# Kernel optimization log

Hardware: AMD Instinct MI355X
Metric: run time of the kernel (lower is better)

## Reference

```python
import jax, jax.numpy as jnp
import numpy as np

INPUT_SIZE = 512
HIDDEN_SIZE = 512
BATCH = 16384


def setup_inputs() -> dict:
    key = jax.random.key(0)
    ks = jax.random.split(key, 11)
    stdv = 1.0 / np.sqrt(HIDDEN_SIZE)
    in_dim = INPUT_SIZE + HIDDEN_SIZE

    def unif(k, shape):
        return jax.random.uniform(k, shape, jnp.float32, -stdv, stdv)

    inp = {
        "input_": jax.random.normal(ks[0], (BATCH, INPUT_SIZE), jnp.float32),
        "prev_h": jax.random.normal(ks[1], (BATCH, HIDDEN_SIZE), jnp.float32),
        "prev_c": jax.random.normal(ks[2], (BATCH, HIDDEN_SIZE), jnp.float32),
        # gate weights in torch nn.Linear layout: (out=hidden, in=input+hidden)
        "W_i": unif(ks[3], (HIDDEN_SIZE, in_dim)),
        "b_i": unif(ks[4], (HIDDEN_SIZE,)),
        "W_f": unif(ks[5], (HIDDEN_SIZE, in_dim)),
        "b_f": unif(ks[6], (HIDDEN_SIZE,)),
        "W_g": unif(ks[7], (HIDDEN_SIZE, in_dim)),
        "b_g": unif(ks[8], (HIDDEN_SIZE,)),
        "W_o": unif(ks[9], (HIDDEN_SIZE, in_dim)),
        "b_o": unif(ks[10], (HIDDEN_SIZE,)),
    }
    return inp


def reference(input_, prev_h, prev_c, W_i, b_i, W_f, b_f, W_g, b_g, W_o, b_o):
    # x_stack = cat((prev_h, input_), dim=1)  -> (batch, hidden+input)
    x_stack = jnp.concatenate([prev_h, input_], axis=1)
    # Fuse the four gate GEMMs into one: stack weights along out dim.
    W = jnp.concatenate([W_i, W_f, W_o, W_g], axis=0)          # (4H, H+I)
    b = jnp.concatenate([b_i, b_f, b_o, b_g], axis=0)          # (4H,)
    gates = x_stack @ W.T + b                                   # (batch, 4H)
    H = prev_h.shape[1]
    i = jax.nn.sigmoid(gates[:, 0 * H:1 * H])
    f = jax.nn.sigmoid(gates[:, 1 * H:2 * H])
    o = jax.nn.sigmoid(gates[:, 2 * H:3 * H])
    g = jnp.tanh(gates[:, 3 * H:4 * H])
    c = f * prev_c + i * g
    h = jnp.tanh(c) * o
    return (h, c)
```

## Files before the change

kernel.cpp:

```cpp
#include <hip/hip_runtime.h>
#include <hip/hip_bf16.h>
#include <math.h>

typedef unsigned short u16;

#define BATCH 16384
#define HID   512
#define KDIM  1024
#define BM    128
#define BN    32
#define BK    64

typedef __bf16 bf16x8 __attribute__((ext_vector_type(8)));
typedef float  floatx4 __attribute__((ext_vector_type(4)));

__device__ __forceinline__ void async_copy16(const void* g, void* l) {
  __builtin_amdgcn_global_load_lds(
      (const __attribute__((address_space(1))) void*)g,
      (__attribute__((address_space(3))) void*)l, 16, 0, 0);
}

__device__ __forceinline__ float fast_sigmoid(float x) {
  return 1.0f / (1.0f + __expf(-x));
}
__device__ __forceinline__ float fast_tanh(float x) {
  float e = __expf(-2.0f * fabsf(x));
  float t = (1.0f - e) / (1.0f + e);
  return x >= 0.0f ? t : -t;
}
__device__ __forceinline__ u16 f2bf(float f) {
  return __builtin_bit_cast(u16, __float2bfloat16(f));
}

__global__ __launch_bounds__(256) void pack_kernel(
    const float* __restrict__ input_, const float* __restrict__ prev_h,
    const float* __restrict__ Wi, const float* __restrict__ Wf,
    const float* __restrict__ Wo, const float* __restrict__ Wg,
    u16* __restrict__ Xb, u16* __restrict__ Wb) {
  int blk = blockIdx.x;
  int col = threadIdx.x * 4;
  const float* src;
  u16* dst;
  if (blk < BATCH) {
    src = (col < HID) ? (prev_h + (size_t)blk * HID + col)
                      : (input_ + (size_t)blk * HID + (col - HID));
    dst = Xb + (size_t)blk * KDIM + col;
  } else {
    int grow = blk - BATCH;
    int gate = grow >> 9;
    int n = grow & (HID - 1);
    const float* s = gate == 0 ? Wi : gate == 1 ? Wf : gate == 2 ? Wo : Wg;
    src = s + (size_t)n * KDIM + col;
    dst = Wb + (size_t)grow * KDIM + col;
  }
  float4 v = *(const float4*)src;
  ushort4 o;
  o.x = f2bf(v.x); o.y = f2bf(v.y); o.z = f2bf(v.z); o.w = f2bf(v.w);
  *(ushort4*)dst = o;
}

__global__ __launch_bounds__(256) void lstm_gemm_kernel(
    const u16* __restrict__ Xb, const u16* __restrict__ Wb,
    const float* __restrict__ Bi, const float* __restrict__ Bf,
    const float* __restrict__ Bo, const float* __restrict__ Bg,
    const float* __restrict__ prevC, float* __restrict__ out) {
  __shared__ u16 lds[16384];

  const int tid = threadIdx.x;
  const int wave = tid >> 6, lane = tid & 63;
  const int lrow = lane & 15, lquad = lane >> 4;
  const int m_block = blockIdx.x * BM;
  const int n_block = blockIdx.y * BN;
  const int m_off = (wave >> 1) * 64;
  const int n_off = (wave & 1) * 16;

  const int swz = ((lane & 7) ^ (lane >> 3)) * 8;
  const u16* gp[8];
  u16* lp[8];
#pragma unroll
  for (int i = 0; i < 8; ++i) {
    int li = wave * 8 + i;
    if (li < 16) {
      int row = m_block + li * 8 + (lane >> 3);
      gp[i] = Xb + (size_t)row * KDIM + swz;
      lp[i] = &lds[li * 512];
    } else {
      int br = (li - 16) * 8 + (lane >> 3);
      int grow = (br >> 5) * HID + n_block + (br & 31);
      gp[i] = Wb + (size_t)grow * KDIM + swz;
      lp[i] = &lds[8192 + (li - 16) * 512];
    }
  }

  floatx4 acc[4][4];
#pragma unroll
  for (int g = 0; g < 4; ++g)
#pragma unroll
    for (int mt = 0; mt < 4; ++mt)
      acc[g][mt] = (floatx4){0.f, 0.f, 0.f, 0.f};

  const int rswz = (lrow & 7);

  for (int k0 = 0; k0 < KDIM; k0 += BK) {
    __syncthreads();
#pragma unroll
    for (int i = 0; i < 8; ++i)
      async_copy16(gp[i] + k0, lp[i]);
    __syncthreads();

#pragma unroll
    for (int kk = 0; kk < 2; ++kk) {
      const int c = kk * 4 + lquad;
      const int ak = (c ^ rswz) * 8;
      bf16x8 a[4], b[4];
#pragma unroll
      for (int mt = 0; mt < 4; ++mt)
        a[mt] = *(const bf16x8*)&lds[(m_off + mt * 16 + lrow) * 64 + ak];
#pragma unroll
      for (int g = 0; g < 4; ++g)
        b[g] = *(const bf16x8*)&lds[8192 + (g * 32 + n_off + lrow) * 64 + ak];
#pragma unroll
      for (int g = 0; g < 4; ++g)
#pragma unroll
        for (int mt = 0; mt < 4; ++mt)
          acc[g][mt] = __builtin_amdgcn_mfma_f32_16x16x32_bf16(
              a[mt], b[g], acc[g][mt], 0, 0, 0);
    }
  }

  const int j = n_block + n_off + lrow;
  const float vbi = Bi[j], vbf = Bf[j], vbo = Bo[j], vbg = Bg[j];
  float* outH = out;
  float* outC = out + (size_t)BATCH * HID;
#pragma unroll
  for (int mt = 0; mt < 4; ++mt) {
    int rowb = m_block + m_off + mt * 16 + lquad * 4;
#pragma unroll
    for (int r = 0; r < 4; ++r) {
      int row = rowb + r;
      float gi = fast_sigmoid(acc[0][mt][r] + vbi);
      float gf = fast_sigmoid(acc[1][mt][r] + vbf);
      float go = fast_sigmoid(acc[2][mt][r] + vbo);
      float gg = fast_tanh(acc[3][mt][r] + vbg);
      float c = gf * prevC[row * HID + j] + gi * gg;
      float h = fast_tanh(c) * go;
      outH[row * HID + j] = h;
      outC[row * HID + j] = c;
    }
  }
}

__global__ void lstm_fallback_kernel(
    const float* __restrict__ input_, const float* __restrict__ prev_h,
    const float* __restrict__ prevC,
    const float* __restrict__ Wi, const float* __restrict__ Bi,
    const float* __restrict__ Wf, const float* __restrict__ Bf,
    const float* __restrict__ Wo, const float* __restrict__ Bo,
    const float* __restrict__ Wg, const float* __restrict__ Bg,
    float* __restrict__ out) {
  int idx = blockIdx.x * blockDim.x + threadIdx.x;
  int b = idx / HID, j = idx % HID;
  if (b >= BATCH) return;
  float si = 0.f, sf = 0.f, so = 0.f, sg = 0.f;
  for (int k = 0; k < KDIM; ++k) {
    float x = (k < HID) ? prev_h[b * HID + k] : input_[b * HID + (k - HID)];
    si += x * Wi[j * KDIM + k];
    sf += x * Wf[j * KDIM + k];
    so += x * Wo[j * KDIM + k];
    sg += x * Wg[j * KDIM + k];
  }
  float gi = fast_sigmoid(si + Bi[j]);
  float gf = fast_sigmoid(sf + Bf[j]);
  float go = fast_sigmoid(so + Bo[j]);
  float gg = fast_tanh(sg + Bg[j]);
  float c = gf * prevC[b * HID + j] + gi * gg;
  out[b * HID + j] = fast_tanh(c) * go;
  out[(size_t)BATCH * HID + b * HID + j] = c;
}

extern "C" void kernel_launch(void* const* d_in, const int* in_sizes, int n_in,
                              void* d_out, int out_size, void* d_ws, size_t ws_size,
                              hipStream_t stream) {
  const float* input_ = (const float*)d_in[0];
  const float* prev_h = (const float*)d_in[1];
  const float* prev_c = (const float*)d_in[2];
  const float* W_i = (const float*)d_in[3];
  const float* b_i = (const float*)d_in[4];
  const float* W_f = (const float*)d_in[5];
  const float* b_f = (const float*)d_in[6];
  const float* W_g = (const float*)d_in[7];
  const float* b_g = (const float*)d_in[8];
  const float* W_o = (const float*)d_in[9];
  const float* b_o = (const float*)d_in[10];
  float* out = (float*)d_out;

  const size_t ws_needed =
      (size_t)BATCH * KDIM * sizeof(u16) + (size_t)4 * HID * KDIM * sizeof(u16);

  if (ws_size < ws_needed) {
    int total = BATCH * HID;
    lstm_fallback_kernel<<<(total + 255) / 256, 256, 0, stream>>>(
        input_, prev_h, prev_c, W_i, b_i, W_f, b_f, W_o, b_o, W_g, b_g, out);
    return;
  }

  u16* Xb = (u16*)d_ws;
  u16* Wb = Xb + (size_t)BATCH * KDIM;

  pack_kernel<<<BATCH + 4 * HID, 256, 0, stream>>>(input_, prev_h,
                                                   W_i, W_f, W_o, W_g, Xb, Wb);

  dim3 grid(BATCH / BM, HID / BN);
  lstm_gemm_kernel<<<grid, 256, 0, stream>>>(Xb, Wb, b_i, b_f, b_o, b_g,
                                             prev_c, out);
}
```

Baseline: 244.7 us.

## Enlarge GEMM tiles to 256x64 per gate with double-buffered LDS pipeline

The LSTM GEMM kernel now uses 512-thread blocks covering 256 batch rows by 64 hidden columns per gate, with BK reduced to 32. The LDS is split into two buffers so async global-to-LDS copies for the next k-slice are issued before computing the current one, overlapping loads with MFMA work. Larger tiles raise data reuse per block and cut the grid size. The cost is higher register pressure (32 accumulator tiles per wave), a new swizzle pattern and fewer blocks per CU.

Result: no change. 248.6 us (+1.6%).

```diff
diff --git a/kernel.cpp b/kernel.cpp
--- a/kernel.cpp
+++ b/kernel.cpp
@@ -7,9 +7,9 @@
 #define BATCH 16384
 #define HID   512
 #define KDIM  1024
-#define BM    128
-#define BN    32
-#define BK    64
+#define BM    256
+#define BNG   64
+#define BK    32
 
 typedef __bf16 bf16x8 __attribute__((ext_vector_type(8)));
 typedef float  floatx4 __attribute__((ext_vector_type(4)));
@@ -59,93 +59,109 @@
   *(ushort4*)dst = o;
 }
 
-__global__ __launch_bounds__(256) void lstm_gemm_kernel(
+__global__ __launch_bounds__(512, 2) void lstm_gemm_kernel(
     const u16* __restrict__ Xb, const u16* __restrict__ Wb,
     const float* __restrict__ Bi, const float* __restrict__ Bf,
     const float* __restrict__ Bo, const float* __restrict__ Bg,
     const float* __restrict__ prevC, float* __restrict__ out) {
-  __shared__ u16 lds[16384];
+  __shared__ u16 lds[2][16384];
 
   const int tid = threadIdx.x;
   const int wave = tid >> 6, lane = tid & 63;
   const int lrow = lane & 15, lquad = lane >> 4;
   const int m_block = blockIdx.x * BM;
-  const int n_block = blockIdx.y * BN;
+  const int nb = blockIdx.y * BNG;
   const int m_off = (wave >> 1) * 64;
-  const int n_off = (wave & 1) * 16;
-
-  const int swz = ((lane & 7) ^ (lane >> 3)) * 8;
-  const u16* gp[8];
-  u16* lp[8];
-#pragma unroll
-  for (int i = 0; i < 8; ++i) {
-    int li = wave * 8 + i;
-    if (li < 16) {
-      int row = m_block + li * 8 + (lane >> 3);
-      gp[i] = Xb + (size_t)row * KDIM + swz;
-      lp[i] = &lds[li * 512];
+  const int n_off = (wave & 1) * 32;
+
+  const int swz = (((lane & 3) ^ ((lane >> 2) & 3)) * 8);
+  const u16* gp[4];
+  int lp[4];
+#pragma unroll
+  for (int i = 0; i < 4; ++i) {
+    int base = wave * 32 + (i & 1) * 16;
+    int r = base + (lane >> 2);
+    if (i < 2) {
+      gp[i] = Xb + (size_t)(m_block + r) * KDIM + swz;
+      lp[i] = base * 32;
     } else {
-      int br = (li - 16) * 8 + (lane >> 3);
-      int grow = (br >> 5) * HID + n_block + (br & 31);
-      gp[i] = Wb + (size_t)grow * KDIM + swz;
-      lp[i] = &lds[8192 + (li - 16) * 512];
+      int gate = r >> 6, col = r & 63;
+      gp[i] = Wb + (size_t)(gate * HID + nb + col) * KDIM + swz;
+      lp[i] = 8192 + base * 32;
     }
   }
 
-  floatx4 acc[4][4];
+  floatx4 acc[4][2][4];
 #pragma unroll
   for (int g = 0; g < 4; ++g)
 #pragma unroll
+    for (int nt = 0; nt < 2; ++nt)
+#pragma unroll
+      for (int mt = 0; mt < 4; ++mt)
+        acc[g][nt][mt] = (floatx4){0.f, 0.f, 0.f, 0.f};
+
+  const int roff = ((lquad ^ (lrow & 3)) * 8);
+
+  auto fill = [&](int buf, int k0) {
+#pragma unroll
+    for (int i = 0; i < 4; ++i)
+      async_copy16(gp[i] + k0, &lds[0][0] + buf * 16384 + lp[i]);
+  };
+
+  auto compute = [&](int buf) {
+    const u16* LA = &lds[buf][0];
+    const u16* LB = &lds[buf][8192];
+    bf16x8 a[4], b[4][2];
+#pragma unroll
     for (int mt = 0; mt < 4; ++mt)
-      acc[g][mt] = (floatx4){0.f, 0.f, 0.f, 0.f};
-
-  const int rswz = (lrow & 7);
-
-  for (int k0 = 0; k0 < KDIM; k0 += BK) {
+      a[mt] = *(const bf16x8*)&LA[(m_off + mt * 16 + lrow) * 32 + roff];
+#pragma unroll
+    for (int g = 0; g < 4; ++g)
+#pragma unroll
+      for (int nt = 0; nt < 2; ++nt)
+        b[g][nt] = *(const bf16x8*)
+            &LB[(g * 64 + n_off + nt * 16 + lrow) * 32 + roff];
+#pragma unroll
+    for (int g = 0; g < 4; ++g)
+#pragma unroll
+      for (int nt = 0; nt < 2; ++nt)
+#pragma unroll
+        for (int mt = 0; mt < 4; ++mt)
+          acc[g][nt][mt] = __builtin_amdgcn_mfma_f32_16x16x32_bf16(
+              a[mt], b[g][nt], acc[g][nt][mt], 0, 0, 0);
+  };
+
+  fill(0, 0);
+  for (int k0 = 0; k0 < KDIM; k0 += 2 * BK) {
     __syncthreads();
-#pragma unroll
-    for (int i = 0; i < 8; ++i)
-      async_copy16(gp[i] + k0, lp[i]);
+    fill(1, k0 + BK);
+    compute(0);
     __syncthreads();
-
-#pragma unroll
-    for (int kk = 0; kk < 2; ++kk) {
-      const int c = kk * 4 + lquad;
-      const int ak = (c ^ rswz) * 8;
-      bf16x8 a[4], b[4];
-#pragma unroll
-      for (int mt = 0; mt < 4; ++mt)
-        a[mt] = *(const bf16x8*)&lds[(m_off + mt * 16 + lrow) * 64 + ak];
-#pragma unroll
-      for (int g = 0; g < 4; ++g)
-        b[g] = *(const bf16x8*)&lds[8192 + (g * 32 + n_off + lrow) * 64 + ak];
-#pragma unroll
-      for (int g = 0; g < 4; ++g)
-#pragma unroll
-        for (int mt = 0; mt < 4; ++mt)
-          acc[g][mt] = __builtin_amdgcn_mfma_f32_16x16x32_bf16(
-              a[mt], b[g], acc[g][mt], 0, 0, 0);
-    }
-  }
-
-  const int j = n_block + n_off + lrow;
-  const float vbi = Bi[j], vbf = Bf[j], vbo = Bo[j], vbg = Bg[j];
+    if (k0 + 2 * BK < KDIM) fill(0, k0 + 2 * BK);
+    compute(1);
+  }
+
   float* outH = out;
   float* outC = out + (size_t)BATCH * HID;
 #pragma unroll
-  for (int mt = 0; mt < 4; ++mt) {
-    int rowb = m_block + m_off + mt * 16 + lquad * 4;
-#pragma unroll
-    for (int r = 0; r < 4; ++r) {
-      int row = rowb + r;
-      float gi = fast_sigmoid(acc[0][mt][r] + vbi);
-      float gf = fast_sigmoid(acc[1][mt][r] + vbf);
-      float go = fast_sigmoid(acc[2][mt][r] + vbo);
-      float gg = fast_tanh(acc[3][mt][r] + vbg);
-      float c = gf * prevC[row * HID + j] + gi * gg;
-      float h = fast_tanh(c) * go;
-      outH[row * HID + j] = h;
-      outC[row * HID + j] = c;
+  for (int nt = 0; nt < 2; ++nt) {
+    const int j = nb + n_off + nt * 16 + lrow;
+    const float vbi = Bi[j], vbf = Bf[j], vbo = Bo[j], vbg = Bg[j];
+#pragma unroll
+    for (int mt = 0; mt < 4; ++mt) {
+      int rowb = m_block + m_off + mt * 16 + lquad * 4;
+#pragma unroll
+      for (int r = 0; r < 4; ++r) {
+        int row = rowb + r;
+        float gi = fast_sigmoid(acc[0][nt][mt][r] + vbi);
+        float gf = fast_sigmoid(acc[1][nt][mt][r] + vbf);
+        float go = fast_sigmoid(acc[2][nt][mt][r] + vbo);
+        float gg = fast_tanh(acc[3][nt][mt][r] + vbg);
+        float c = gf * prevC[row * HID + j] + gi * gg;
+        float h = fast_tanh(c) * go;
+        outH[row * HID + j] = h;
+        outC[row * HID + j] = c;
+      }
     }
   }
 }
@@ -210,7 +226,7 @@
   pack_kernel<<<BATCH + 4 * HID, 256, 0, stream>>>(input_, prev_h,
                                                    W_i, W_f, W_o, W_g, Xb, Wb);
 
-  dim3 grid(BATCH / BM, HID / BN);
-  lstm_gemm_kernel<<<grid, 256, 0, stream>>>(Xb, Wb, b_i, b_f, b_o, b_g,
+  dim3 grid(BATCH / BM, HID / BNG);
+  lstm_gemm_kernel<<<grid, 512, 0, stream>>>(Xb, Wb, b_i, b_f, b_o, b_g,
                                              prev_c, out);
 }
```

## Pre-swizzle weights into MFMA fragment layout and double-buffer A tiles

Applied to the files above, without the earlier changes.

The pack kernel now writes bf16 weights in an MFMA-fragment-ordered layout, so each wave loads B operands directly from global memory into registers instead of staging them through LDS. The GEMM kernel moves to 512-thread blocks covering 128 rows by 128 hidden columns across all four gates, with each wave owning a 16-column slice and 8 M tiles. Only the X tile goes through LDS, now double-buffered so the next K step's copy overlaps the current MFMA work. The cost is much higher register pressure (128 accumulator floats plus prefetched B fragments) and heavy reliance on L2 for weight reuse across blocks.

Result: no change. 241.1 us (-1.4%).

```diff
diff --git a/kernel.cpp b/kernel.cpp
--- a/kernel.cpp
+++ b/kernel.cpp
@@ -8,8 +8,8 @@
 #define HID   512
 #define KDIM  1024
 #define BM    128
-#define BN    32
-#define BK    64
+#define BNG   128
+#define NSTEP 16
 
 typedef __bf16 bf16x8 __attribute__((ext_vector_type(8)));
 typedef float  floatx4 __attribute__((ext_vector_type(4)));
@@ -34,107 +34,117 @@
 
 __global__ __launch_bounds__(256) void pack_kernel(
     const float* __restrict__ input_, const float* __restrict__ prev_h,
-    const float* __restrict__ Wi, const float* __restrict__ Wf,
+    const float* __restrict__ Wi, const float* __restrict__ Wf_,
     const float* __restrict__ Wo, const float* __restrict__ Wg,
-    u16* __restrict__ Xb, u16* __restrict__ Wb) {
+    u16* __restrict__ Xb, u16* __restrict__ Wf) {
   int blk = blockIdx.x;
-  int col = threadIdx.x * 4;
-  const float* src;
-  u16* dst;
+  int k = threadIdx.x * 4;
   if (blk < BATCH) {
-    src = (col < HID) ? (prev_h + (size_t)blk * HID + col)
-                      : (input_ + (size_t)blk * HID + (col - HID));
-    dst = Xb + (size_t)blk * KDIM + col;
+    const float* src = (k < HID) ? (prev_h + (size_t)blk * HID + k)
+                                 : (input_ + (size_t)blk * HID + (k - HID));
+    float4 v = *(const float4*)src;
+    ushort4 o;
+    o.x = f2bf(v.x); o.y = f2bf(v.y); o.z = f2bf(v.z); o.w = f2bf(v.w);
+    *(ushort4*)(Xb + (size_t)blk * KDIM + k) = o;
   } else {
     int grow = blk - BATCH;
-    int gate = grow >> 9;
+    int g = grow >> 9;
     int n = grow & (HID - 1);
-    const float* s = gate == 0 ? Wi : gate == 1 ? Wf : gate == 2 ? Wo : Wg;
-    src = s + (size_t)n * KDIM + col;
-    dst = Wb + (size_t)grow * KDIM + col;
-  }
-  float4 v = *(const float4*)src;
-  ushort4 o;
-  o.x = f2bf(v.x); o.y = f2bf(v.y); o.z = f2bf(v.z); o.w = f2bf(v.w);
-  *(ushort4*)dst = o;
-}
-
-__global__ __launch_bounds__(256) void lstm_gemm_kernel(
-    const u16* __restrict__ Xb, const u16* __restrict__ Wb,
+    const float* s = g == 0 ? Wi : g == 1 ? Wf_ : g == 2 ? Wo : Wg;
+    float4 v = *(const float4*)(s + (size_t)n * KDIM + k);
+    ushort4 o;
+    o.x = f2bf(v.x); o.y = f2bf(v.y); o.z = f2bf(v.z); o.w = f2bf(v.w);
+    size_t d = ((size_t)((g * 32 + (n >> 4)) * 32 + (k >> 5)) * 64 +
+                ((k >> 3) & 3) * 16 + (n & 15)) * 8 + (k & 7);
+    *(ushort4*)(Wf + d) = o;
+  }
+}
+
+__global__ __launch_bounds__(512, 2) void lstm_gemm_kernel(
+    const u16* __restrict__ Xb, const u16* __restrict__ Wf,
     const float* __restrict__ Bi, const float* __restrict__ Bf,
     const float* __restrict__ Bo, const float* __restrict__ Bg,
     const float* __restrict__ prevC, float* __restrict__ out) {
-  __shared__ u16 lds[16384];
+  __shared__ u16 lds[2][8192];
 
   const int tid = threadIdx.x;
   const int wave = tid >> 6, lane = tid & 63;
   const int lrow = lane & 15, lquad = lane >> 4;
   const int m_block = blockIdx.x * BM;
-  const int n_block = blockIdx.y * BN;
-  const int m_off = (wave >> 1) * 64;
-  const int n_off = (wave & 1) * 16;
-
-  const int swz = ((lane & 7) ^ (lane >> 3)) * 8;
-  const u16* gp[8];
-  u16* lp[8];
-#pragma unroll
-  for (int i = 0; i < 8; ++i) {
-    int li = wave * 8 + i;
-    if (li < 16) {
-      int row = m_block + li * 8 + (lane >> 3);
-      gp[i] = Xb + (size_t)row * KDIM + swz;
-      lp[i] = &lds[li * 512];
-    } else {
-      int br = (li - 16) * 8 + (lane >> 3);
-      int grow = (br >> 5) * HID + n_block + (br & 31);
-      gp[i] = Wb + (size_t)grow * KDIM + swz;
-      lp[i] = &lds[8192 + (li - 16) * 512];
+  const int ntg = blockIdx.y * 8 + wave;
+
+  const int swz = ((lane & 7) ^ ((lane >> 3) & 7)) * 8;
+  const u16* gp[2];
+  int lp[2];
+#pragma unroll
+  for (int i = 0; i < 2; ++i) {
+    int li = wave * 2 + i;
+    gp[i] = Xb + (size_t)(m_block + li * 8 + (lane >> 3)) * KDIM + swz;
+    lp[i] = li * 512;
+  }
+
+  floatx4 acc[4][8];
+#pragma unroll
+  for (int g = 0; g < 4; ++g)
+#pragma unroll
+    for (int mt = 0; mt < 8; ++mt)
+      acc[g][mt] = (floatx4){0.f, 0.f, 0.f, 0.f};
+
+  auto fill = [&](int buf, int S) {
+#pragma unroll
+    for (int i = 0; i < 2; ++i)
+      async_copy16(gp[i] + S * 64, &lds[0][0] + buf * 8192 + lp[i]);
+  };
+
+  auto loadB = [&](int S, bf16x8 (&dst)[2][4]) {
+#pragma unroll
+    for (int kk = 0; kk < 2; ++kk)
+#pragma unroll
+      for (int g = 0; g < 4; ++g)
+        dst[kk][g] = *(const bf16x8*)(
+            Wf + (((size_t)(g * 32 + ntg) * 32 + (S * 2 + kk)) << 9) +
+            lane * 8);
+  };
+
+  auto compute = [&](int buf, bf16x8 (&B)[2][4]) {
+    const u16* LA = &lds[buf][0];
+#pragma unroll
+    for (int kk = 0; kk < 2; ++kk) {
+#pragma unroll
+      for (int mt = 0; mt < 8; ++mt) {
+        bf16x8 a = *(const bf16x8*)
+            &LA[(mt * 16 + lrow) * 64 + (((kk * 4 + lquad) ^ (lrow & 7)) * 8)];
+#pragma unroll
+        for (int g = 0; g < 4; ++g)
+          acc[g][mt] = __builtin_amdgcn_mfma_f32_16x16x32_bf16(
+              a, B[kk][g], acc[g][mt], 0, 0, 0);
+      }
     }
-  }
-
-  floatx4 acc[4][4];
-#pragma unroll
-  for (int g = 0; g < 4; ++g)
-#pragma unroll
-    for (int mt = 0; mt < 4; ++mt)
-      acc[g][mt] = (floatx4){0.f, 0.f, 0.f, 0.f};
-
-  const int rswz = (lrow & 7);
-
-  for (int k0 = 0; k0 < KDIM; k0 += BK) {
+  };
+
+  bf16x8 b0[2][4], b1[2][4];
+  loadB(0, b0);
+  fill(0, 0);
+  for (int S = 0; S < NSTEP; S += 2) {
     __syncthreads();
-#pragma unroll
-    for (int i = 0; i < 8; ++i)
-      async_copy16(gp[i] + k0, lp[i]);
+    fill(1, S + 1);
+    loadB(S + 1 < NSTEP ? S + 1 : S, b1);
+    compute(0, b0);
     __syncthreads();
-
-#pragma unroll
-    for (int kk = 0; kk < 2; ++kk) {
-      const int c = kk * 4 + lquad;
-      const int ak = (c ^ rswz) * 8;
-      bf16x8 a[4], b[4];
-#pragma unroll
-      for (int mt = 0; mt < 4; ++mt)
-        a[mt] = *(const bf16x8*)&lds[(m_off + mt * 16 + lrow) * 64 + ak];
-#pragma unroll
-      for (int g = 0; g < 4; ++g)
-        b[g] = *(const bf16x8*)&lds[8192 + (g * 32 + n_off + lrow) * 64 + ak];
-#pragma unroll
-      for (int g = 0; g < 4; ++g)
-#pragma unroll
-        for (int mt = 0; mt < 4; ++mt)
-          acc[g][mt] = __builtin_amdgcn_mfma_f32_16x16x32_bf16(
-              a[mt], b[g], acc[g][mt], 0, 0, 0);
+    if (S + 2 < NSTEP) {
+      fill(0, S + 2);
+      loadB(S + 2, b0);
     }
-  }
-
-  const int j = n_block + n_off + lrow;
+    compute(1, b1);
+  }
+
+  const int j = ntg * 16 + lrow;
   const float vbi = Bi[j], vbf = Bf[j], vbo = Bo[j], vbg = Bg[j];
   float* outH = out;
   float* outC = out + (size_t)BATCH * HID;
 #pragma unroll
-  for (int mt = 0; mt < 4; ++mt) {
-    int rowb = m_block + m_off + mt * 16 + lquad * 4;
+  for (int mt = 0; mt < 8; ++mt) {
+    int rowb = m_block + mt * 16 + lquad * 4;
 #pragma unroll
     for (int r = 0; r < 4; ++r) {
       int row = rowb + r;
@@ -205,12 +215,12 @@
   }
 
   u16* Xb = (u16*)d_ws;
-  u16* Wb = Xb + (size_t)BATCH * KDIM;
+  u16* Wf = Xb + (size_t)BATCH * KDIM;
 
   pack_kernel<<<BATCH + 4 * HID, 256, 0, stream>>>(input_, prev_h,
-                                                   W_i, W_f, W_o, W_g, Xb, Wb);
-
-  dim3 grid(BATCH / BM, HID / BN);
-  lstm_gemm_kernel<<<grid, 256, 0, stream>>>(Xb, Wb, b_i, b_f, b_o, b_g,
+                                                   W_i, W_f, W_o, W_g, Xb, Wf);
+
+  dim3 grid(BATCH / BM, HID / BNG);
+  lstm_gemm_kernel<<<grid, 512, 0, stream>>>(Xb, Wf, b_i, b_f, b_o, b_g,
                                              prev_c, out);
 }
```
